# Kernel optimization log

Hardware: AMD Instinct MI355X
Metric: run time of the kernel (lower is better)

The kernel has to match this reference:

```python
import jax, jax.numpy as jnp
import numpy as np

DIM = 512        # token feature dim
HID = 1024       # expert hidden dim (dim * 2)
E = 16           # num_experts
N = 8192         # num tokens
TOPK = 2         # experts active per token (routing sparsity)


def setup_inputs() -> dict:
    key = jax.random.key(0)
    k_x, k_s, k_w1, k_w2 = jax.random.split(key, 4)
    x = jax.random.normal(k_x, (N, DIM), dtype=jnp.float32)
    # sparse routing scores: top-2 experts per token get nonzero score, rest 0
    scores = jax.random.uniform(k_s, (N, E), dtype=jnp.float32)
    vals, idx = jax.lax.top_k(scores, TOPK)
    routing_tensor = jnp.zeros((N, E), jnp.float32).at[jnp.arange(N)[:, None], idx].set(vals)
    # per-expert MLP params (depth=2, bias=True): Linear(DIM->HID), GELU, Linear(HID->DIM)
    W1 = jax.random.normal(k_w1, (E, DIM, HID), dtype=jnp.float32) * (1.0 / np.sqrt(DIM))
    b1 = jnp.zeros((E, HID), jnp.float32)
    W2 = jax.random.normal(k_w2, (E, HID, DIM), dtype=jnp.float32) * (1.0 / np.sqrt(HID))
    b2 = jnp.zeros((E, DIM), jnp.float32)
    return {"x": x, "routing_tensor": routing_tensor, "W1": W1, "b1": b1, "W2": W2, "b2": b2}


def reference(x, routing_tensor, W1, b1, W2, b2):
    # out[n] = sum_e routing[n,e] * MLP_e(x[n]); rows with score 0 contribute 0,
    # which is exactly the original mask-gather / scatter-add semantics.
    h = jax.nn.gelu(jnp.einsum('nd,edh->enh', x, W1) + b1[:, None, :], approximate=False)
    y = jnp.einsum('enh,ehd->end', h, W2) + b2[:, None, :]  # [E, N, DIM]
    return jnp.einsum('end,ne->nd', y, routing_tensor)       # combine weighted by scores
```

## Files before the change

kernel.cpp:

```cpp
#include <hip/hip_runtime.h>
#include <hip/hip_bf16.h>

#define NTOK 8192
#define DIM 512
#define HID 1024
#define NE 16
#define CAP 1280

typedef __attribute__((ext_vector_type(8))) short short8;
typedef __attribute__((ext_vector_type(4))) float f32x4;

static __device__ __forceinline__ unsigned short f2bf(float f) {
    __hip_bfloat16 h = __float2bfloat16(f);
    return __builtin_bit_cast(unsigned short, h);
}

static __device__ __forceinline__ void gl_lds16(const unsigned short* g, unsigned short* l) {
    __builtin_amdgcn_global_load_lds(
        (const __attribute__((address_space(1))) unsigned int*)g,
        (__attribute__((address_space(3))) unsigned int*)l, 16, 0, 0);
}

static __device__ __forceinline__ float gelu_f(float v) {
    float u = v * (0.7978845608f + 0.0356774081f * v * v);
    return v / (1.0f + __expf(-2.0f * u));
}

__global__ void transpose_cvt(const float* __restrict__ src, unsigned short* __restrict__ dst,
                              int R, int C) {
    __shared__ float tile[32][33];
    int e = blockIdx.z;
    src += (size_t)e * R * C;
    dst += (size_t)e * R * C;
    int c0 = blockIdx.x * 32, r0 = blockIdx.y * 32;
    int tx = threadIdx.x, ty = threadIdx.y;
    #pragma unroll
    for (int i = 0; i < 32; i += 8)
        tile[ty + i][tx] = src[(size_t)(r0 + ty + i) * C + c0 + tx];
    __syncthreads();
    #pragma unroll
    for (int i = 0; i < 32; i += 8)
        dst[(size_t)(c0 + ty + i) * R + r0 + tx] = f2bf(tile[tx][ty + i]);
}

__global__ void route_fill(const float* __restrict__ routing, int* __restrict__ cnt,
                           int* __restrict__ sidx, float* __restrict__ wtb) {
    int n = blockIdx.x * blockDim.x + threadIdx.x;
    if (n >= NTOK) return;
    int slot = 0;
    #pragma unroll
    for (int e = 0; e < NE; e++) {
        float r = routing[n * NE + e];
        if (r != 0.0f) {
            if (slot < 2) {
                int pos = atomicAdd(&cnt[e], 1);
                if (pos < CAP) {
                    sidx[e * CAP + pos] = n * 2 + slot;
                    wtb[e * CAP + pos] = r;
                }
            }
            slot++;
        }
    }
}

__global__ void gather_x(const float* __restrict__ x, const int* __restrict__ cnt,
                         const int* __restrict__ sidx, unsigned short* __restrict__ xg) {
    int b = blockIdx.x;
    int e = b / CAP, row = b - e * CAP;
    int t = threadIdx.x;
    int c = cnt[e]; c = c > CAP ? CAP : c;
    ushort4 o;
    if (row < c) {
        int n = sidx[b] >> 1;
        float4 v = ((const float4*)(x + (size_t)n * DIM))[t];
        o.x = f2bf(v.x); o.y = f2bf(v.y); o.z = f2bf(v.z); o.w = f2bf(v.w);
    } else {
        o.x = 0; o.y = 0; o.z = 0; o.w = 0;
    }
    ((ushort4*)(xg + (size_t)b * DIM))[t] = o;
}

template <int K>
__device__ __forceinline__ void mfma_main(const unsigned short* __restrict__ A,
                                          const unsigned short* __restrict__ B,
                                          unsigned short* As, unsigned short* Bs,
                                          f32x4 acc[4][4]) {
    int t = threadIdx.x;
    int wave = t >> 6, lane = t & 63;
    int wm = wave >> 1, wn = wave & 1;
    int quad = lane >> 4, l16 = lane & 15;
    int lr = lane >> 3;
    int col = (lane & 7) << 3;
    for (int kc = 0; kc < K; kc += 64) {
        __syncthreads();
        #pragma unroll
        for (int j = 0; j < 4; j++) {
            int rb = wave * 32 + j * 8;
            gl_lds16(A + (size_t)(rb + lr) * K + kc + col, As + rb * 64);
            gl_lds16(B + (size_t)(rb + lr) * K + kc + col, Bs + rb * 64);
        }
        __syncthreads();
        #pragma unroll
        for (int kk = 0; kk < 64; kk += 32) {
            short8 av[4], bv[4];
            #pragma unroll
            for (int mt = 0; mt < 4; mt++)
                av[mt] = *(const short8*)(&As[(wm * 64 + mt * 16 + l16) * 64 + kk + quad * 8]);
            #pragma unroll
            for (int nt = 0; nt < 4; nt++)
                bv[nt] = *(const short8*)(&Bs[(wn * 64 + nt * 16 + l16) * 64 + kk + quad * 8]);
            #pragma unroll
            for (int mt = 0; mt < 4; mt++)
                #pragma unroll
                for (int nt = 0; nt < 4; nt++)
                    acc[mt][nt] = __builtin_amdgcn_mfma_f32_16x16x32_bf16(
                        av[mt], bv[nt], acc[mt][nt], 0, 0, 0);
        }
    }
}

__global__ __launch_bounds__(256) void gemm1_gelu(
    const unsigned short* __restrict__ xg, const unsigned short* __restrict__ w1t,
    const float* __restrict__ b1, const int* __restrict__ cnt,
    unsigned short* __restrict__ hbuf) {
    __shared__ __align__(16) unsigned short As[128 * 64];
    __shared__ __align__(16) unsigned short Bs[128 * 64];
    int e = blockIdx.z;
    int c = cnt[e]; c = c > CAP ? CAP : c;
    int m0 = blockIdx.y * 128;
    if (m0 >= c) return;
    int n0 = blockIdx.x * 128;
    const unsigned short* A = xg + ((size_t)e * CAP + m0) * DIM;
    const unsigned short* B = w1t + ((size_t)e * HID + n0) * DIM;
    f32x4 z = {0.f, 0.f, 0.f, 0.f};
    f32x4 acc[4][4];
    #pragma unroll
    for (int mt = 0; mt < 4; mt++)
        #pragma unroll
        for (int nt = 0; nt < 4; nt++) acc[mt][nt] = z;
    mfma_main<DIM>(A, B, As, Bs, acc);
    int t = threadIdx.x;
    int wave = t >> 6, lane = t & 63;
    int wm = wave >> 1, wn = wave & 1, quad = lane >> 4, l16 = lane & 15;
    #pragma unroll
    for (int nt = 0; nt < 4; nt++) {
        int gn = n0 + wn * 64 + nt * 16 + l16;
        float bias = b1[e * HID + gn];
        #pragma unroll
        for (int mt = 0; mt < 4; mt++) {
            #pragma unroll
            for (int r = 0; r < 4; r++) {
                int gm = m0 + wm * 64 + mt * 16 + quad * 4 + r;
                float v = acc[mt][nt][r] + bias;
                hbuf[((size_t)e * CAP + gm) * HID + gn] = f2bf(gelu_f(v));
            }
        }
    }
}

__global__ __launch_bounds__(256) void gemm2_store(
    const unsigned short* __restrict__ hbuf, const unsigned short* __restrict__ w2t,
    const float* __restrict__ b2, const int* __restrict__ cnt,
    const int* __restrict__ sidx, const float* __restrict__ wtb,
    float* __restrict__ ybuf) {
    __shared__ __align__(16) unsigned short As[128 * 64];
    __shared__ __align__(16) unsigned short Bs[128 * 64];
    int e = blockIdx.z;
    int c = cnt[e]; c = c > CAP ? CAP : c;
    int m0 = blockIdx.y * 128;
    if (m0 >= c) return;
    int n0 = blockIdx.x * 128;
    const unsigned short* A = hbuf + ((size_t)e * CAP + m0) * HID;
    const unsigned short* B = w2t + ((size_t)e * DIM + n0) * HID;
    f32x4 z = {0.f, 0.f, 0.f, 0.f};
    f32x4 acc[4][4];
    #pragma unroll
    for (int mt = 0; mt < 4; mt++)
        #pragma unroll
        for (int nt = 0; nt < 4; nt++) acc[mt][nt] = z;
    mfma_main<HID>(A, B, As, Bs, acc);
    int t = threadIdx.x;
    int wave = t >> 6, lane = t & 63;
    int wm = wave >> 1, wn = wave & 1, quad = lane >> 4, l16 = lane & 15;
    #pragma unroll
    for (int mt = 0; mt < 4; mt++) {
        #pragma unroll
        for (int r = 0; r < 4; r++) {
            int gm = m0 + wm * 64 + mt * 16 + quad * 4 + r;
            if (gm < c) {
                int si = sidx[e * CAP + gm];
                float wgt = wtb[e * CAP + gm];
                float* yrow = ybuf + (size_t)si * DIM;
                #pragma unroll
                for (int nt = 0; nt < 4; nt++) {
                    int gn = n0 + wn * 64 + nt * 16 + l16;
                    yrow[gn] = wgt * (acc[mt][nt][r] + b2[e * DIM + gn]);
                }
            }
        }
    }
}

__global__ void combine(const float* __restrict__ yb, float* __restrict__ out) {
    int i = blockIdx.x * 256 + threadIdx.x;
    int n = i >> 7, d4 = i & 127;
    float4 a = ((const float4*)(yb + (size_t)(2 * n) * DIM))[d4];
    float4 b = ((const float4*)(yb + (size_t)(2 * n + 1) * DIM))[d4];
    float4 o;
    o.x = a.x + b.x; o.y = a.y + b.y; o.z = a.z + b.z; o.w = a.w + b.w;
    ((float4*)(out + (size_t)n * DIM))[d4] = o;
}

extern "C" void kernel_launch(void* const* d_in, const int* in_sizes, int n_in,
                              void* d_out, int out_size, void* d_ws, size_t ws_size,
                              hipStream_t stream) {
    const float* x       = (const float*)d_in[0];
    const float* routing = (const float*)d_in[1];
    const float* W1      = (const float*)d_in[2];
    const float* b1      = (const float*)d_in[3];
    const float* W2      = (const float*)d_in[4];
    const float* b2      = (const float*)d_in[5];
    float* out = (float*)d_out;

    char* w = (char*)d_ws;
    int*   cnt  = (int*)w;
    int*   sidx = (int*)(w + 256);
    float* wtb  = (float*)(w + 256 + NE * CAP * 4);
    char* base = w + 256 + NE * CAP * 8;
    unsigned short* xg  = (unsigned short*)base;
    unsigned short* hb  = xg + (size_t)NE * CAP * DIM;
    unsigned short* w1t = hb + (size_t)NE * CAP * HID;
    unsigned short* w2t = w1t + (size_t)NE * HID * DIM;
    float* ybuf = (float*)(w2t + (size_t)NE * DIM * HID);

    hipMemsetAsync(cnt, 0, 256, stream);

    transpose_cvt<<<dim3(HID / 32, DIM / 32, NE), dim3(32, 8), 0, stream>>>(W1, w1t, DIM, HID);
    transpose_cvt<<<dim3(DIM / 32, HID / 32, NE), dim3(32, 8), 0, stream>>>(W2, w2t, HID, DIM);

    route_fill<<<NTOK / 256, 256, 0, stream>>>(routing, cnt, sidx, wtb);
    gather_x<<<NE * CAP, 128, 0, stream>>>(x, cnt, sidx, xg);

    gemm1_gelu<<<dim3(HID / 128, CAP / 128, NE), 256, 0, stream>>>(xg, w1t, b1, cnt, hb);
    gemm2_store<<<dim3(DIM / 128, CAP / 128, NE), 256, 0, stream>>>(hb, w2t, b2, cnt, sidx, wtb, ybuf);
    combine<<<(NTOK * DIM / 4) / 256, 256, 0, stream>>>(ybuf, out);
}
```

Before: 274.5 us.

## Double-buffer gemm2 LDS, merge weight transposes, aggregate routing atomics per block

The second expert GEMM now uses a double-buffered LDS main loop that issues the next K-chunk's global-to-LDS loads before computing on the current chunk, so load latency is hidden behind MFMA work. The two weight transpose-convert launches are merged into one launch. The routing kernel now counts tokens per expert in shared memory and issues one global atomic per expert per block instead of one per token. The cost is doubled LDS for gemm2, which may lower occupancy, and the slot assignment order within an expert changes.

```diff
diff --git a/kernel.cpp b/kernel.cpp
--- a/kernel.cpp
+++ b/kernel.cpp
@@ -26,13 +26,22 @@
     return v / (1.0f + __expf(-2.0f * u));
 }
 
-__global__ void transpose_cvt(const float* __restrict__ src, unsigned short* __restrict__ dst,
-                              int R, int C) {
+__global__ void transpose_cvt2(const float* __restrict__ W1, const float* __restrict__ W2,
+                               unsigned short* __restrict__ w1t, unsigned short* __restrict__ w2t) {
     __shared__ float tile[32][33];
-    int e = blockIdx.z;
-    src += (size_t)e * R * C;
-    dst += (size_t)e * R * C;
-    int c0 = blockIdx.x * 32, r0 = blockIdx.y * 32;
+    int b = blockIdx.x;
+    const float* src; unsigned short* dst; int R, C, bx, by;
+    if (b < 8192) {
+        int e = b >> 9, rem = b & 511; bx = rem & 31; by = rem >> 5;
+        R = DIM; C = HID;
+        src = W1 + (size_t)e * R * C; dst = w1t + (size_t)e * R * C;
+    } else {
+        int bb = b - 8192;
+        int e = bb >> 9, rem = bb & 511; bx = rem & 15; by = rem >> 4;
+        R = HID; C = DIM;
+        src = W2 + (size_t)e * R * C; dst = w2t + (size_t)e * R * C;
+    }
+    int c0 = bx * 32, r0 = by * 32;
     int tx = threadIdx.x, ty = threadIdx.y;
     #pragma unroll
     for (int i = 0; i < 32; i += 8)
@@ -43,24 +52,32 @@
         dst[(size_t)(c0 + ty + i) * R + r0 + tx] = f2bf(tile[tx][ty + i]);
 }
 
-__global__ void route_fill(const float* __restrict__ routing, int* __restrict__ cnt,
-                           int* __restrict__ sidx, float* __restrict__ wtb) {
-    int n = blockIdx.x * blockDim.x + threadIdx.x;
-    if (n >= NTOK) return;
-    int slot = 0;
+__global__ __launch_bounds__(256) void route_fill(const float* __restrict__ routing,
+                                                  int* __restrict__ cnt,
+                                                  int* __restrict__ sidx,
+                                                  float* __restrict__ wtb) {
+    __shared__ int lcnt[NE], lbase[NE];
+    int t = threadIdx.x;
+    int n = blockIdx.x * 256 + t;
+    if (t < NE) lcnt[t] = 0;
+    __syncthreads();
+    int mye[2]; float myw[2]; int mypos[2]; int slot = 0;
     #pragma unroll
     for (int e = 0; e < NE; e++) {
         float r = routing[n * NE + e];
-        if (r != 0.0f) {
-            if (slot < 2) {
-                int pos = atomicAdd(&cnt[e], 1);
-                if (pos < CAP) {
-                    sidx[e * CAP + pos] = n * 2 + slot;
-                    wtb[e * CAP + pos] = r;
-                }
-            }
+        if (r != 0.0f && slot < 2) {
+            mye[slot] = e; myw[slot] = r;
+            mypos[slot] = atomicAdd(&lcnt[e], 1);
             slot++;
         }
+    }
+    __syncthreads();
+    if (t < NE) lbase[t] = atomicAdd(&cnt[t], lcnt[t]);
+    __syncthreads();
+    for (int s = 0; s < slot; s++) {
+        int e = mye[s];
+        int p = lbase[e] + mypos[s];
+        if (p < CAP) { sidx[e * CAP + p] = n * 2 + s; wtb[e * CAP + p] = myw[s]; }
     }
 }
 
@@ -117,6 +134,56 @@
                     acc[mt][nt] = __builtin_amdgcn_mfma_f32_16x16x32_bf16(
                         av[mt], bv[nt], acc[mt][nt], 0, 0, 0);
         }
+    }
+}
+
+template <int K>
+__device__ __forceinline__ void mfma_main_db(const unsigned short* __restrict__ A,
+                                             const unsigned short* __restrict__ B,
+                                             unsigned short (*As)[128 * 64],
+                                             unsigned short (*Bs)[128 * 64],
+                                             f32x4 acc[4][4]) {
+    int t = threadIdx.x;
+    int wave = t >> 6, lane = t & 63;
+    int wm = wave >> 1, wn = wave & 1;
+    int quad = lane >> 4, l16 = lane & 15;
+    int lr = lane >> 3;
+    int col = (lane & 7) << 3;
+    #pragma unroll
+    for (int j = 0; j < 4; j++) {
+        int rb = wave * 32 + j * 8;
+        gl_lds16(A + (size_t)(rb + lr) * K + col, As[0] + rb * 64);
+        gl_lds16(B + (size_t)(rb + lr) * K + col, Bs[0] + rb * 64);
+    }
+    __syncthreads();
+    int cur = 0;
+    for (int kc = 64; kc <= K; kc += 64) {
+        if (kc < K) {
+            #pragma unroll
+            for (int j = 0; j < 4; j++) {
+                int rb = wave * 32 + j * 8;
+                gl_lds16(A + (size_t)(rb + lr) * K + kc + col, As[cur ^ 1] + rb * 64);
+                gl_lds16(B + (size_t)(rb + lr) * K + kc + col, Bs[cur ^ 1] + rb * 64);
+            }
+        }
+        #pragma unroll
+        for (int kk = 0; kk < 64; kk += 32) {
+            short8 av[4], bv[4];
+            #pragma unroll
+            for (int mt = 0; mt < 4; mt++)
+                av[mt] = *(const short8*)(&As[cur][(wm * 64 + mt * 16 + l16) * 64 + kk + quad * 8]);
+            #pragma unroll
+            for (int nt = 0; nt < 4; nt++)
+                bv[nt] = *(const short8*)(&Bs[cur][(wn * 64 + nt * 16 + l16) * 64 + kk + quad * 8]);
+            #pragma unroll
+            for (int mt = 0; mt < 4; mt++)
+                #pragma unroll
+                for (int nt = 0; nt < 4; nt++)
+                    acc[mt][nt] = __builtin_amdgcn_mfma_f32_16x16x32_bf16(
+                        av[mt], bv[nt], acc[mt][nt], 0, 0, 0);
+        }
+        __syncthreads();
+        cur ^= 1;
     }
 }
 
@@ -164,8 +231,8 @@
     const float* __restrict__ b2, const int* __restrict__ cnt,
     const int* __restrict__ sidx, const float* __restrict__ wtb,
     float* __restrict__ ybuf) {
-    __shared__ __align__(16) unsigned short As[128 * 64];
-    __shared__ __align__(16) unsigned short Bs[128 * 64];
+    __shared__ __align__(16) unsigned short As[2][128 * 64];
+    __shared__ __align__(16) unsigned short Bs[2][128 * 64];
     int e = blockIdx.z;
     int c = cnt[e]; c = c > CAP ? CAP : c;
     int m0 = blockIdx.y * 128;
@@ -179,7 +246,7 @@
     for (int mt = 0; mt < 4; mt++)
         #pragma unroll
         for (int nt = 0; nt < 4; nt++) acc[mt][nt] = z;
-    mfma_main<HID>(A, B, As, Bs, acc);
+    mfma_main_db<HID>(A, B, As, Bs, acc);
     int t = threadIdx.x;
     int wave = t >> 6, lane = t & 63;
     int wm = wave >> 1, wn = wave & 1, quad = lane >> 4, l16 = lane & 15;
@@ -236,8 +303,7 @@
 
     hipMemsetAsync(cnt, 0, 256, stream);
 
-    transpose_cvt<<<dim3(HID / 32, DIM / 32, NE), dim3(32, 8), 0, stream>>>(W1, w1t, DIM, HID);
-    transpose_cvt<<<dim3(DIM / 32, HID / 32, NE), dim3(32, 8), 0, stream>>>(W2, w2t, HID, DIM);
+    transpose_cvt2<<<16384, dim3(32, 8), 0, stream>>>(W1, W2, w1t, w2t);
 
     route_fill<<<NTOK / 256, 256, 0, stream>>>(routing, cnt, sidx, wtb);
     gather_x<<<NE * CAP, 128, 0, stream>>>(x, cnt, sidx, xg);
```

Result: faster. 254.2 us (-7.4%).
